# Kernel tuning notes

Hardware: AMD Instinct MI355X
Metric: run time of the kernel (lower is better)

Reference implementation:

```python
import jax, jax.numpy as jnp
import numpy as np


def setup_inputs() -> dict:
    key = jax.random.key(0)
    k0, k1, k2, k3, k4 = jax.random.split(key, 5)
    n, c, s, h, w = 4, 128, 31, 32, 22
    x = jax.random.normal(k0, (n, c, s, h, w), dtype=jnp.float32)
    # 1x1 conv to a single channel == per-pixel dot over channels + scalar bias
    scale = 1.0 / np.sqrt(c).astype(np.float32)
    w1 = jax.random.normal(k1, (c,), dtype=jnp.float32) * scale
    b1 = jax.random.normal(k2, (), dtype=jnp.float32) * 0.01
    w2 = jax.random.normal(k3, (c,), dtype=jnp.float32) * scale
    b2 = jax.random.normal(k4, (), dtype=jnp.float32) * 0.01
    return {"x": x, "w1": w1, "b1": b1, "w2": w2, "b2": b2, "top_k": 16}


def reference(x, w1, b1, w2, b2, top_k):
    n, c, s, h, w = x.shape
    hw = h * w
    ns = n * (s - 1)
    # adjacent-frame pairs; 1x1 conv (C->1) as channel contraction
    X0 = jnp.einsum('ncshw,c->nshw', x[:, :, : s - 1], w1) + b1  # (n, s-1, h, w)
    X1 = jnp.einsum('ncshw,c->nshw', x[:, :, 1:], w2) + b2       # (n, s-1, h, w)
    X0 = X0.reshape(ns, hw)
    X1 = X1.reshape(ns, hw)
    # outer-product scores per frame pair, softmax over last dim
    attention = jax.nn.softmax(X0[:, :, None] * X1[:, None, :], axis=2)  # (ns, hw, hw)
    # top-k values along last dim -> (ns, hw, k); torch .view(ns, k, h, w)
    # is a raw row-major reinterpretation, so a plain reshape is faithful.
    vals, _ = jax.lax.top_k(attention, top_k)
    vals = vals.reshape(n, s - 1, top_k, h, w)
    # trans_out: (n, s-1, k, h, w) -> (n, k, s-1, h, w)
    return jnp.transpose(vals, (0, 2, 1, 3, 4))
```

## Files before the change

### kernel.cpp

```cpp
#include <hip/hip_runtime.h>
#include <math.h>

#define NB   4
#define C    128
#define S    31
#define HW   704
#define T    30
#define NS   120
#define K    16
#define NFR  124

__global__ __launch_bounds__(768) void conv_select_kernel(
    const float* __restrict__ x,
    const float* __restrict__ w1, const float* __restrict__ b1p,
    const float* __restrict__ w2, const float* __restrict__ b2p,
    float* __restrict__ A, float* __restrict__ B,
    float* __restrict__ btop, float* __restrict__ bbot) {
  const int tid = threadIdx.x;
  const int wv    = __builtin_amdgcn_readfirstlane(tid) >> 6;
  const int cg    = wv / 3;
  const int local = tid - cg * 192;
  const bool act  = local < 176;
  const int f4    = act ? local : 175;
  const int fr    = blockIdx.x;
  const int sf    = fr % S;
  const int n     = fr / S;

  const float4* xp =
      (const float4*)(x + (((size_t)(n * C + cg * 32) * S + sf) * HW)) + f4;
  float4 a1 = make_float4(0.f, 0.f, 0.f, 0.f);
  float4 a2 = make_float4(0.f, 0.f, 0.f, 0.f);
#pragma unroll
  for (int c = 0; c < 32; ++c) {
    float4 xv = xp[(size_t)c * (S * HW / 4)];
    const float wa = w1[cg * 32 + c];
    const float wb = w2[cg * 32 + c];
    a1.x = fmaf(xv.x, wa, a1.x); a1.y = fmaf(xv.y, wa, a1.y);
    a1.z = fmaf(xv.z, wa, a1.z); a1.w = fmaf(xv.w, wa, a1.w);
    a2.x = fmaf(xv.x, wb, a2.x); a2.y = fmaf(xv.y, wb, a2.y);
    a2.z = fmaf(xv.z, wb, a2.z); a2.w = fmaf(xv.w, wb, a2.w);
  }

  __shared__ float4 s1[4][176];
  __shared__ float4 s2[4][176];
  if (act) {
    s1[cg][f4] = a1;
    s2[cg][f4] = a2;
  }
  __syncthreads();

  if (tid < 176) {
    float4 r1 = s1[0][tid], r2 = s2[0][tid];
#pragma unroll
    for (int u = 1; u < 4; ++u) {
      float4 t1 = s1[u][tid], t2 = s2[u][tid];
      r1.x += t1.x; r1.y += t1.y; r1.z += t1.z; r1.w += t1.w;
      r2.x += t2.x; r2.y += t2.y; r2.z += t2.z; r2.w += t2.w;
    }
    const float bb1 = b1p[0], bb2 = b2p[0];
    r1.x += bb1; r1.y += bb1; r1.z += bb1; r1.w += bb1;
    r2.x += bb2; r2.y += bb2; r2.z += bb2; r2.w += bb2;
    if (sf < T)
      ((float4*)(A + (size_t)(n * T + sf) * HW))[tid] = r1;
    if (sf >= 1)
      ((float4*)(B + (size_t)(n * T + sf - 1) * HW))[tid] = r2;
    s2[0][tid] = r2;
  }
  __syncthreads();

  if (tid < 64 && sf >= 1) {
    const int i = n * T + sf - 1;
    const float* bs = (const float*)&s2[0][0];
    float vt[11], vb[11];
#pragma unroll
    for (int j = 0; j < 11; ++j) {
      const float v = bs[j * 64 + tid];
      vt[j] = v;
      vb[j] = v;
    }
#pragma unroll 1
    for (int r = 0; r < K; ++r) {
      float lmT = vt[0], lmB = vb[0];
#pragma unroll
      for (int j = 1; j < 11; ++j) {
        lmT = fmaxf(lmT, vt[j]);
        lmB = fminf(lmB, vb[j]);
      }
      float gT = lmT, gB = lmB;
#pragma unroll
      for (int off = 1; off < 64; off <<= 1) {
        gT = fmaxf(gT, __shfl_xor(gT, off, 64));
        gB = fminf(gB, __shfl_xor(gB, off, 64));
      }
      const unsigned long long mT = __ballot(lmT == gT);
      const unsigned long long mB = __ballot(lmB == gB);
      if (tid == (int)(__ffsll(mT) - 1)) {
        bool done = false;
#pragma unroll
        for (int j = 0; j < 11; ++j) {
          const bool hit = (!done) && (vt[j] == gT);
          vt[j] = hit ? -INFINITY : vt[j];
          done  = done || hit;
        }
      }
      if (tid == (int)(__ffsll(mB) - 1)) {
        bool done = false;
#pragma unroll
        for (int j = 0; j < 11; ++j) {
          const bool hit = (!done) && (vb[j] == gB);
          vb[j] = hit ? INFINITY : vb[j];
          done  = done || hit;
        }
      }
      if (tid == 0) {
        btop[i * K + r] = gT;
        bbot[i * K + r] = gB;
      }
    }
  }
}

__global__ __launch_bounds__(256) void softmax_topk_kernel(
    const float* __restrict__ A, const float* __restrict__ B,
    const float* __restrict__ btop, const float* __restrict__ bbot,
    float* __restrict__ out) {
  __shared__ float4 bs4[176];
  __shared__ float  partial[4][64];
  __shared__ float  seltop[K], selbot[K];
  const int tid  = threadIdx.x;
  const int lane = tid & 63;
  const int w    = tid >> 6;
  const int i    = blockIdx.x / 11;
  const int slab = blockIdx.x % 11;
  const int n    = i / T;
  const int tp   = i % T;

  if (tid < 176) bs4[tid] = ((const float4*)(B + i * HW))[tid];
  if (tid >= 176 && tid < 176 + K) {
    seltop[tid - 176] = btop[i * K + (tid - 176)];
    selbot[tid - 176] = bbot[i * K + (tid - 176)];
  }

  const int   r   = slab * 64 + lane;
  const float a   = A[i * HW + r];
  const float st0 = btop[i * K];
  const float sb0 = bbot[i * K];
  const float L2E = 1.4426950408889634f;
  const float a2  = a * L2E;
  const float nm  = -((a >= 0.f) ? a * st0 : a * sb0) * L2E;
  __syncthreads();

  float p0 = 0.f, p1 = 0.f, p2 = 0.f, p3 = 0.f;
#pragma unroll 11
  for (int j = 0; j < 44; ++j) {
    const float4 bq = bs4[w * 44 + j];
    p0 += __builtin_amdgcn_exp2f(fmaf(a2, bq.x, nm));
    p1 += __builtin_amdgcn_exp2f(fmaf(a2, bq.y, nm));
    p2 += __builtin_amdgcn_exp2f(fmaf(a2, bq.z, nm));
    p3 += __builtin_amdgcn_exp2f(fmaf(a2, bq.w, nm));
  }
  partial[w][lane] = (p0 + p1) + (p2 + p3);
  __syncthreads();

  if (w == 0) {
    const float part =
        (partial[0][lane] + partial[1][lane]) +
        (partial[2][lane] + partial[3][lane]);
    const float rp = 1.f / part;
    float ov[16];
#pragma unroll
    for (int t = 0; t < K; ++t) {
      const float sel = (a >= 0.f) ? seltop[t] : selbot[t];
      ov[t] = __builtin_amdgcn_exp2f(fmaf(a2, sel, nm)) * rp;
    }
    float* op = out + (((size_t)(n * K + r / 44)) * T + tp) * HW + (r % 44) * K;
#pragma unroll
    for (int t4 = 0; t4 < 4; ++t4)
      ((float4*)op)[t4] = ((const float4*)ov)[t4];
  }
}

extern "C" void kernel_launch(void* const* d_in, const int* in_sizes, int n_in,
                              void* d_out, int out_size, void* d_ws, size_t ws_size,
                              hipStream_t stream) {
  (void)in_sizes; (void)n_in; (void)out_size; (void)ws_size;
  const float* x  = (const float*)d_in[0];
  const float* w1 = (const float*)d_in[1];
  const float* b1 = (const float*)d_in[2];
  const float* w2 = (const float*)d_in[3];
  const float* b2 = (const float*)d_in[4];
  float* out = (float*)d_out;

  float* A    = (float*)d_ws;
  float* B    = A + NS * HW;
  float* btop = B + NS * HW;
  float* bbot = btop + NS * K;

  conv_select_kernel<<<NFR, 768, 0, stream>>>(x, w1, b1, w2, b2,
                                              A, B, btop, bbot);
  softmax_topk_kernel<<<NS * 11, 256, 0, stream>>>(A, B, btop, bbot, out);
}
```

Measured before the change: 107.9 us.

## Split conv across more blocks and move top-k selection into softmax kernel

```diff
diff --git a/kernel.cpp b/kernel.cpp
--- a/kernel.cpp
+++ b/kernel.cpp
@@ -8,23 +8,20 @@
 #define T    30
 #define NS   120
 #define K    16
-#define NFR  124
 
-__global__ __launch_bounds__(768) void conv_select_kernel(
+__global__ __launch_bounds__(256) void conv_kernel(
     const float* __restrict__ x,
     const float* __restrict__ w1, const float* __restrict__ b1p,
     const float* __restrict__ w2, const float* __restrict__ b2p,
-    float* __restrict__ A, float* __restrict__ B,
-    float* __restrict__ btop, float* __restrict__ bbot) {
-  const int tid = threadIdx.x;
-  const int wv    = __builtin_amdgcn_readfirstlane(tid) >> 6;
-  const int cg    = wv / 3;
-  const int local = tid - cg * 192;
-  const bool act  = local < 176;
-  const int f4    = act ? local : 175;
-  const int fr    = blockIdx.x;
-  const int sf    = fr % S;
-  const int n     = fr / S;
+    float* __restrict__ A, float* __restrict__ B) {
+  const int tid  = threadIdx.x;
+  const int lane = tid & 63;
+  const int cg   = tid >> 6;
+  const int g    = blockIdx.x * 64 + lane;
+  const int fr   = g / 176;
+  const int f4   = g % 176;
+  const int sf   = fr % S;
+  const int n    = fr / S;
 
   const float4* xp =
       (const float4*)(x + (((size_t)(n * C + cg * 32) * S + sf) * HW)) + f4;
@@ -40,16 +37,12 @@
     a2.x = fmaf(xv.x, wb, a2.x); a2.y = fmaf(xv.y, wb, a2.y);
     a2.z = fmaf(xv.z, wb, a2.z); a2.w = fmaf(xv.w, wb, a2.w);
   }
-
-  __shared__ float4 s1[4][176];
-  __shared__ float4 s2[4][176];
-  if (act) {
-    s1[cg][f4] = a1;
-    s2[cg][f4] = a2;
-  }
+  __shared__ float4 s1[4][64];
+  __shared__ float4 s2[4][64];
+  s1[cg][lane] = a1;
+  s2[cg][lane] = a2;
   __syncthreads();
-
-  if (tid < 176) {
+  if (tid < 64) {
     float4 r1 = s1[0][tid], r2 = s2[0][tid];
 #pragma unroll
     for (int u = 1; u < 4; ++u) {
@@ -61,16 +54,33 @@
     r1.x += bb1; r1.y += bb1; r1.z += bb1; r1.w += bb1;
     r2.x += bb2; r2.y += bb2; r2.z += bb2; r2.w += bb2;
     if (sf < T)
-      ((float4*)(A + (size_t)(n * T + sf) * HW))[tid] = r1;
+      ((float4*)(A + (size_t)(n * T + sf) * HW))[f4] = r1;
     if (sf >= 1)
-      ((float4*)(B + (size_t)(n * T + sf - 1) * HW))[tid] = r2;
-    s2[0][tid] = r2;
+      ((float4*)(B + (size_t)(n * T + sf - 1) * HW))[f4] = r2;
   }
+}
+
+__global__ __launch_bounds__(256) void softmax_select_kernel(
+    const float* __restrict__ A, const float* __restrict__ B,
+    float* __restrict__ out) {
+  __shared__ float4 bs4[176];
+  __shared__ float  partial[4][64];
+  __shared__ float  seltop[K], selbot[K];
+  const int tid  = threadIdx.x;
+  const int lane = tid & 63;
+  const int w    = tid >> 6;
+  const int i    = blockIdx.x / 11;
+  const int slab = blockIdx.x % 11;
+  const int n    = i / T;
+  const int tp   = i % T;
+
+  if (tid < 176) bs4[tid] = ((const float4*)(B + i * HW))[tid];
+  const int   r = slab * 64 + lane;
+  const float a = A[i * HW + r];
   __syncthreads();
 
-  if (tid < 64 && sf >= 1) {
-    const int i = n * T + sf - 1;
-    const float* bs = (const float*)&s2[0][0];
+  if (tid < 64) {
+    const float* bs = (const float*)&bs4[0];
     float vt[11], vb[11];
 #pragma unroll
     for (int j = 0; j < 11; ++j) {
@@ -79,7 +89,7 @@
       vb[j] = v;
     }
 #pragma unroll 1
-    for (int r = 0; r < K; ++r) {
+    for (int rr = 0; rr < K; ++rr) {
       float lmT = vt[0], lmB = vb[0];
 #pragma unroll
       for (int j = 1; j < 11; ++j) {
@@ -113,42 +123,18 @@
         }
       }
       if (tid == 0) {
-        btop[i * K + r] = gT;
-        bbot[i * K + r] = gB;
+        seltop[rr] = gT;
+        selbot[rr] = gB;
       }
     }
   }
-}
+  __syncthreads();
 
-__global__ __launch_bounds__(256) void softmax_topk_kernel(
-    const float* __restrict__ A, const float* __restrict__ B,
-    const float* __restrict__ btop, const float* __restrict__ bbot,
-    float* __restrict__ out) {
-  __shared__ float4 bs4[176];
-  __shared__ float  partial[4][64];
-  __shared__ float  seltop[K], selbot[K];
-  const int tid  = threadIdx.x;
-  const int lane = tid & 63;
-  const int w    = tid >> 6;
-  const int i    = blockIdx.x / 11;
-  const int slab = blockIdx.x % 11;
-  const int n    = i / T;
-  const int tp   = i % T;
-
-  if (tid < 176) bs4[tid] = ((const float4*)(B + i * HW))[tid];
-  if (tid >= 176 && tid < 176 + K) {
-    seltop[tid - 176] = btop[i * K + (tid - 176)];
-    selbot[tid - 176] = bbot[i * K + (tid - 176)];
-  }
-
-  const int   r   = slab * 64 + lane;
-  const float a   = A[i * HW + r];
-  const float st0 = btop[i * K];
-  const float sb0 = bbot[i * K];
+  const float st0 = seltop[0];
+  const float sb0 = selbot[0];
   const float L2E = 1.4426950408889634f;
   const float a2  = a * L2E;
   const float nm  = -((a >= 0.f) ? a * st0 : a * sb0) * L2E;
-  __syncthreads();
 
   float p0 = 0.f, p1 = 0.f, p2 = 0.f, p3 = 0.f;
 #pragma unroll 11
@@ -191,12 +177,9 @@
   const float* b2 = (const float*)d_in[4];
   float* out = (float*)d_out;
 
-  float* A    = (float*)d_ws;
-  float* B    = A + NS * HW;
-  float* btop = B + NS * HW;
-  float* bbot = btop + NS * K;
+  float* A = (float*)d_ws;
+  float* B = A + NS * HW;
 
-  conv_select_kernel<<<NFR, 768, 0, stream>>>(x, w1, b1, w2, b2,
-                                              A, B, btop, bbot);
-  softmax_topk_kernel<<<NS * 11, 256, 0, stream>>>(A, B, btop, bbot, out);
+  conv_kernel<<<341, 256, 0, stream>>>(x, w1, b1, w2, b2, A, B);
+  softmax_select_kernel<<<NS * 11, 256, 0, stream>>>(A, B, out);
 }
```

Result: no change. 109.5 us (+1.5%).
